# Performance work log

Hardware: AMD Instinct MI355X
Metric: run time of the kernel (lower is better)

The kernel has to match this reference:

```python
import jax, jax.numpy as jnp
import numpy as np

N = 256
IL_MMI = 0.02      # insertion loss MMI
IMB = 0.01         # imbalance MMI
IL_CR = 0.02       # insertion loss Crossing
CT = 0.01          # cross talk Crossing


def _mmi_matrix():
    # 2x2 MMI: sqrt(1-IL)*[[t, i r],[i r, t]] with t=sqrt((1+imb)/2), r=sqrt((1-imb)/2)
    a = np.sqrt(1.0 - IL_MMI)
    t = np.sqrt((1.0 + IMB) / 2.0)
    r = np.sqrt((1.0 - IMB) / 2.0)
    mmi2 = a * np.array([[t, 1j * r], [1j * r, t]], dtype=np.complex64)
    # block-diagonal over even pairs (0,1),(2,3),...
    return jnp.asarray(np.kron(np.eye(N // 2, dtype=np.complex64), mmi2))


def _crossing_matrix():
    # pairs start at odd index 1; rows 0 and N-1 pass through with amplitude sqrt(1-IL)*sqrt(1-CT)
    a = np.sqrt(1.0 - IL_CR)
    thru = a * np.sqrt(1.0 - CT)
    cr2 = a * np.array([[np.sqrt(CT), 1j * np.sqrt(1.0 - CT)],
                        [1j * np.sqrt(1.0 - CT), np.sqrt(CT)]], dtype=np.complex64)
    M = np.zeros((N, N), dtype=np.complex64)
    M[0, 0] = thru
    for i in range(1, N - 1, 2):
        M[i:i + 2, i:i + 2] = cr2
    if N % 2 == 0:
        M[-1, -1] = thru
    return jnp.asarray(M)


def setup_inputs() -> dict:
    key = jax.random.key(0)
    thetas = jax.random.uniform(key, (N // 2 + 2, N), dtype=jnp.float32) * (2.0 * np.pi)
    return {"thetas": thetas}


def reference(thetas):
    MMI = _mmi_matrix()
    CR = _crossing_matrix()
    phases = jnp.exp(1j * thetas)  # [N//2+2, N] complex64; diag phase-shift layers

    # arch = ht[0] @ I  (diagonal left-multiply == row scaling)
    arch0 = jnp.diag(phases[0])

    def body(arch, ph):
        # one mesh stage with trailing crossing (iterations i = 0 .. N//2-2)
        arch = MMI @ arch
        arch = ph[:, None] * arch      # ht[i+1] @ arch
        arch = MMI @ arch
        arch = CR @ arch
        return arch, None

    arch, _ = jax.lax.scan(body, arch0, phases[1:N // 2])

    # last loop iteration (i = N//2-1): no crossing
    arch = MMI @ arch
    arch = phases[N // 2][:, None] * arch
    arch = MMI @ arch
    # final phase layer ht[N//2+1]
    arch = phases[N // 2 + 1][:, None] * arch
    return arch
```

## Files before the change

kernel.cpp:

```cpp
#include <hip/hip_runtime.h>


__device__ __forceinline__ float dpp_up1(float x) {
    return __int_as_float(__builtin_amdgcn_update_dpp(
        __float_as_int(x), __float_as_int(x), 0x138, 0xf, 0xf, false));
}
__device__ __forceinline__ float dpp_dn1(float x) {
    return __int_as_float(__builtin_amdgcn_update_dpp(
        __float_as_int(x), __float_as_int(x), 0x130, 0xf, 0xf, false));
}

__device__ __forceinline__ void sincos4(float4 th, float sn[4], float cs[4]) {
    __sincosf(th.x, &sn[0], &cs[0]);
    __sincosf(th.y, &sn[1], &cs[1]);
    __sincosf(th.z, &sn[2], &cs[2]);
    __sincosf(th.w, &sn[3], &cs[3]);
}

struct Coef {
    float Er[2], Ei[2], Fr[2], Fi[2], Gr[2], Gi[2];
};

__global__ __launch_bounds__(64, 1)
void neuropuls_mesh_kernel(const float* __restrict__ thetas,
                           float* __restrict__ out)
{
    constexpr int N = 256;
    const int lane = threadIdx.x;
    const int col  = blockIdx.x;

    const float U  = 0.98f * 0.505f;
    const float W  = 0.98f * 0.495f;
    const float Gc = 0.98f * sqrtf(0.505f * 0.495f);
    const float BT = sqrtf(0.98f * 0.01f);
    const float BR = sqrtf(0.98f * 0.99f);

    float vr[4] = {0.f, 0.f, 0.f, 0.f};
    float vi[4] = {0.f, 0.f, 0.f, 0.f};

    {
        const float th0 = thetas[col];
        float s0, c0;
        __sincosf(th0, &s0, &c0);
        const int r0 = col - 4 * lane;
        if (0 <= r0 && r0 < 4) { vr[r0] = c0; vi[r0] = s0; }
    }

    const float* tp = thetas + N + 4 * lane;

    auto prep4 = [&](float4 th, Coef& K) {
        float s[4], c[4];
        sincos4(th, s, c);
        #pragma unroll
        for (int p = 0; p < 2; ++p) {
            const float c0 = c[2 * p], c1 = c[2 * p + 1];
            const float s0 = s[2 * p], s1 = s[2 * p + 1];
            K.Er[p] = U * c0 - W * c1;   K.Ei[p] = U * s0 - W * s1;
            K.Fr[p] = U * c1 - W * c0;   K.Fi[p] = U * s1 - W * s0;
            K.Gr[p] = -Gc * (s0 + s1);   K.Gi[p] = Gc * (c0 + c1);
        }
    };

    auto mstep = [&](const Coef& K) {
        #pragma unroll
        for (int p = 0; p < 2; ++p) {
            const int x = 2 * p, y = 2 * p + 1;
            const float xr = vr[x], xi = vi[x], yr = vr[y], yi = vi[y];
            vr[x] = K.Er[p] * xr - K.Ei[p] * xi + K.Gr[p] * yr - K.Gi[p] * yi;
            vi[x] = K.Er[p] * xi + K.Ei[p] * xr + K.Gr[p] * yi + K.Gi[p] * yr;
            vr[y] = K.Gr[p] * xr - K.Gi[p] * xi + K.Fr[p] * yr - K.Fi[p] * yi;
            vi[y] = K.Gr[p] * xi + K.Gi[p] * xr + K.Fr[p] * yi + K.Fi[p] * yr;
        }
    };

    auto crossing = [&]() {
        float pv3r = dpp_up1(vr[3]);
        float pv3i = dpp_up1(vi[3]);
        float nv0r = dpp_dn1(vr[0]);
        float nv0i = dpp_dn1(vi[0]);
        {
            float xr = vr[1], xi = vi[1], yr = vr[2], yi = vi[2];
            vr[1] = BT * xr - BR * yi;  vi[1] = BT * xi + BR * yr;
            vr[2] = BT * yr - BR * xi;  vi[2] = BT * yi + BR * xr;
        }
        {
            float yr = vr[0], yi = vi[0];
            float nr = BT * yr - BR * pv3i;
            float ni = BT * yi + BR * pv3r;
            vr[0] = (lane == 0) ? BR * yr : nr;
            vi[0] = (lane == 0) ? BR * yi : ni;
        }
        {
            float xr = vr[3], xi = vi[3];
            float nr = BT * xr - BR * nv0i;
            float ni = BT * xi + BR * nv0r;
            vr[3] = (lane == 63) ? BR * xr : nr;
            vi[3] = (lane == 63) ? BR * xi : ni;
        }
    };

    Coef KA;
    float4 thB, thC;
    {
        float4 t1 = *(const float4*)tp;  tp += N;
        thB       = *(const float4*)tp;  tp += N;
        thC       = *(const float4*)tp;  tp += N;
        prep4(t1, KA);
    }

    #pragma unroll 3
    for (int s = 1; s <= 126; ++s) {
        float4 thD = *(const float4*)tp;  tp += N;
        Coef KB;
        prep4(thB, KB);
        mstep(KA);
        crossing();
        KA = KB;
        thB = thC; thC = thD;
    }

    mstep(KA);
    crossing();

    {
        Coef KF;
        prep4(thB, KF);
        mstep(KF);
        float sn[4], cs[4];
        sincos4(thC, sn, cs);
        #pragma unroll
        for (int j = 0; j < 4; ++j) {
            float r = vr[j], i = vi[j];
            vr[j] = cs[j] * r - sn[j] * i;
            vi[j] = cs[j] * i + sn[j] * r;
        }
    }

    #pragma unroll
    for (int j = 0; j < 4; ++j) {
        const int idx = (4 * lane + j) * N + col;
        out[idx]         = vr[j];
        out[N * N + idx] = vi[j];
    }
}

extern "C" void kernel_launch(void* const* d_in, const int* in_sizes, int n_in,
                              void* d_out, int out_size, void* d_ws, size_t ws_size,
                              hipStream_t stream)
{
    const float* thetas = (const float*)d_in[0];
    float* out = (float*)d_out;
    (void)in_sizes; (void)n_in; (void)out_size; (void)d_ws; (void)ws_size;
    neuropuls_mesh_kernel<<<dim3(256), dim3(64), 0, stream>>>(thetas, out);
}
```

Before: 80.06 us.

## Precompute per-stage MMI coefficients in a separate kernel shared by all columns

Adds a preceding kernel that evaluates the sincos and combined MMI-phase-MMI coefficients once per stage and lane and writes them to workspace. The main kernel then streams these precomputed float4 coefficients instead of recomputing sincos in each of the 256 column blocks. This removes redundant transcendental work per block but adds a second launch and triples the per-step load volume (three float4s instead of one), which becomes a latency-bound dependent load chain in a single-wave-per-block kernel.

```diff
diff --git a/kernel.cpp b/kernel.cpp
--- a/kernel.cpp
+++ b/kernel.cpp
@@ -17,21 +17,44 @@
     __sincosf(th.w, &sn[3], &cs[3]);
 }
 
-struct Coef {
-    float Er[2], Ei[2], Fr[2], Fi[2], Gr[2], Gi[2];
-};
+__global__ __launch_bounds__(64)
+void coef_kernel(const float* __restrict__ thetas,
+                 float* __restrict__ coefs)
+{
+    const int s0   = blockIdx.x;
+    const int lane = threadIdx.x;
+
+    const float U  = 0.98f * 0.505f;
+    const float W  = 0.98f * 0.495f;
+    const float Gc = 0.98f * sqrtf(0.505f * 0.495f);
+
+    float4 th = *(const float4*)(thetas + (s0 + 1) * 256 + 4 * lane);
+    float s[4], c[4];
+    sincos4(th, s, c);
+
+    float4 A, B, C;
+    A.x = U * c[0] - W * c[1];   A.y = U * s[0] - W * s[1];
+    A.z = U * c[1] - W * c[0];   A.w = U * s[1] - W * s[0];
+    B.x = -Gc * (s[0] + s[1]);   B.y = Gc * (c[0] + c[1]);
+    B.z = -Gc * (s[2] + s[3]);   B.w = Gc * (c[2] + c[3]);
+    C.x = U * c[2] - W * c[3];   C.y = U * s[2] - W * s[3];
+    C.z = U * c[3] - W * c[2];   C.w = U * s[3] - W * s[2];
+
+    float4* cp = (float4*)coefs;
+    cp[0 * 8192 + s0 * 64 + lane] = A;
+    cp[1 * 8192 + s0 * 64 + lane] = B;
+    cp[2 * 8192 + s0 * 64 + lane] = C;
+}
 
 __global__ __launch_bounds__(64, 1)
 void neuropuls_mesh_kernel(const float* __restrict__ thetas,
+                           const float* __restrict__ coefs,
                            float* __restrict__ out)
 {
     constexpr int N = 256;
     const int lane = threadIdx.x;
     const int col  = blockIdx.x;
 
-    const float U  = 0.98f * 0.505f;
-    const float W  = 0.98f * 0.495f;
-    const float Gc = 0.98f * sqrtf(0.505f * 0.495f);
     const float BT = sqrtf(0.98f * 0.01f);
     const float BR = sqrtf(0.98f * 0.99f);
 
@@ -46,30 +69,20 @@
         if (0 <= r0 && r0 < 4) { vr[r0] = c0; vi[r0] = s0; }
     }
 
-    const float* tp = thetas + N + 4 * lane;
-
-    auto prep4 = [&](float4 th, Coef& K) {
-        float s[4], c[4];
-        sincos4(th, s, c);
-        #pragma unroll
-        for (int p = 0; p < 2; ++p) {
-            const float c0 = c[2 * p], c1 = c[2 * p + 1];
-            const float s0 = s[2 * p], s1 = s[2 * p + 1];
-            K.Er[p] = U * c0 - W * c1;   K.Ei[p] = U * s0 - W * s1;
-            K.Fr[p] = U * c1 - W * c0;   K.Fi[p] = U * s1 - W * s0;
-            K.Gr[p] = -Gc * (s0 + s1);   K.Gi[p] = Gc * (c0 + c1);
+    auto mstep = [&](const float4 A, const float4 B, const float4 C) {
+        {
+            const float xr = vr[0], xi = vi[0], yr = vr[1], yi = vi[1];
+            vr[0] = A.x * xr - A.y * xi + B.x * yr - B.y * yi;
+            vi[0] = A.x * xi + A.y * xr + B.x * yi + B.y * yr;
+            vr[1] = B.x * xr - B.y * xi + A.z * yr - A.w * yi;
+            vi[1] = B.x * xi + B.y * xr + A.z * yi + A.w * yr;
         }
-    };
-
-    auto mstep = [&](const Coef& K) {
-        #pragma unroll
-        for (int p = 0; p < 2; ++p) {
-            const int x = 2 * p, y = 2 * p + 1;
-            const float xr = vr[x], xi = vi[x], yr = vr[y], yi = vi[y];
-            vr[x] = K.Er[p] * xr - K.Ei[p] * xi + K.Gr[p] * yr - K.Gi[p] * yi;
-            vi[x] = K.Er[p] * xi + K.Ei[p] * xr + K.Gr[p] * yi + K.Gi[p] * yr;
-            vr[y] = K.Gr[p] * xr - K.Gi[p] * xi + K.Fr[p] * yr - K.Fi[p] * yi;
-            vi[y] = K.Gr[p] * xi + K.Gi[p] * xr + K.Fr[p] * yi + K.Fi[p] * yr;
+        {
+            const float xr = vr[2], xi = vi[2], yr = vr[3], yi = vi[3];
+            vr[2] = C.x * xr - C.y * xi + B.z * yr - B.w * yi;
+            vi[2] = C.x * xi + C.y * xr + B.z * yi + B.w * yr;
+            vr[3] = B.z * xr - B.w * xi + C.z * yr - C.w * yi;
+            vi[3] = B.z * xi + B.w * xr + C.z * yi + C.w * yr;
         }
     };
 
@@ -99,35 +112,35 @@
         }
     };
 
-    Coef KA;
-    float4 thB, thC;
-    {
-        float4 t1 = *(const float4*)tp;  tp += N;
-        thB       = *(const float4*)tp;  tp += N;
-        thC       = *(const float4*)tp;  tp += N;
-        prep4(t1, KA);
-    }
+    const float4* pA = (const float4*)coefs + lane;
+    const float4* pB = (const float4*)coefs + 8192 + lane;
+    const float4* pC = (const float4*)coefs + 16384 + lane;
+
+    float4 A0 = pA[0],   B0 = pB[0],   C0 = pC[0];
+    float4 A1 = pA[64],  B1 = pB[64],  C1 = pC[64];
+    float4 A2 = pA[128], B2 = pB[128], C2 = pC[128];
+    pA += 192; pB += 192; pC += 192;
 
     #pragma unroll 3
     for (int s = 1; s <= 126; ++s) {
-        float4 thD = *(const float4*)tp;  tp += N;
-        Coef KB;
-        prep4(thB, KB);
-        mstep(KA);
+        float4 A3 = pA[0], B3 = pB[0], C3 = pC[0];
+        pA += 64; pB += 64; pC += 64;
+        mstep(A0, B0, C0);
         crossing();
-        KA = KB;
-        thB = thC; thC = thD;
+        A0 = A1; B0 = B1; C0 = C1;
+        A1 = A2; B1 = B2; C1 = C2;
+        A2 = A3; B2 = B3; C2 = C3;
     }
 
-    mstep(KA);
+    mstep(A0, B0, C0);
     crossing();
 
+    mstep(A1, B1, C1);
+
     {
-        Coef KF;
-        prep4(thB, KF);
-        mstep(KF);
+        float4 thF = *(const float4*)(thetas + 129 * N + 4 * lane);
         float sn[4], cs[4];
-        sincos4(thC, sn, cs);
+        sincos4(thF, sn, cs);
         #pragma unroll
         for (int j = 0; j < 4; ++j) {
             float r = vr[j], i = vi[j];
@@ -149,7 +162,10 @@
                               hipStream_t stream)
 {
     const float* thetas = (const float*)d_in[0];
-    float* out = (float*)d_out;
-    (void)in_sizes; (void)n_in; (void)out_size; (void)d_ws; (void)ws_size;
-    neuropuls_mesh_kernel<<<dim3(256), dim3(64), 0, stream>>>(thetas, out);
+    float* out   = (float*)d_out;
+    float* coefs = (float*)d_ws;
+    (void)in_sizes; (void)n_in; (void)out_size; (void)ws_size;
+
+    coef_kernel<<<dim3(128), dim3(64), 0, stream>>>(thetas, coefs);
+    neuropuls_mesh_kernel<<<dim3(256), dim3(64), 0, stream>>>(thetas, coefs, out);
 }
```

After: 82.57 us. 3.1% more time.
